# Kernel tuning notes

Hardware: AMD Instinct MI355X
Metric: run time of the kernel (lower is better)

Reference implementation:

```python
import jax, jax.numpy as jnp
import numpy as np

N_NODES = 50000
N_EDGES = 800000
IN_DIM = 256
HIDDEN = 64
HEADS = 4
LATENT = 128


def setup_inputs() -> dict:
    key = jax.random.key(0)
    ks = jax.random.split(key, 16)
    def p(k, shape, scale=0.05):
        return jax.random.normal(k, shape, jnp.float32) * scale
    d = {}
    d["x"] = jax.random.normal(ks[0], (N_NODES, IN_DIM), jnp.float32)
    d["edge_index"] = jax.random.randint(ks[1], (2, N_EDGES), 0, N_NODES)
    d["w_in"] = p(ks[2], (IN_DIM, HIDDEN)); d["b_in"] = jnp.zeros((HIDDEN,), jnp.float32)
    # GAT layer 0: in=HIDDEN, out=HIDDEN, heads=HEADS, concat
    d["W0"] = p(ks[3], (HIDDEN, HEADS * HIDDEN))
    d["as0"] = p(ks[4], (HEADS, HIDDEN)); d["ad0"] = p(ks[5], (HEADS, HIDDEN))
    d["bb0"] = jnp.zeros((HEADS * HIDDEN,), jnp.float32)
    # GAT layer 1: in=HEADS*HIDDEN, out=HIDDEN, heads=HEADS, concat
    d["W1"] = p(ks[6], (HEADS * HIDDEN, HEADS * HIDDEN))
    d["as1"] = p(ks[7], (HEADS, HIDDEN)); d["ad1"] = p(ks[8], (HEADS, HIDDEN))
    d["bb1"] = jnp.zeros((HEADS * HIDDEN,), jnp.float32)
    # GAT layer 2: in=HEADS*HIDDEN, out=HIDDEN, heads=1, concat=False
    d["W2"] = p(ks[9], (HEADS * HIDDEN, HIDDEN))
    d["as2"] = p(ks[10], (1, HIDDEN)); d["ad2"] = p(ks[11], (1, HIDDEN))
    d["bb2"] = jnp.zeros((HIDDEN,), jnp.float32)
    d["w_out"] = p(ks[12], (HIDDEN, LATENT)); d["b_out"] = jnp.zeros((LATENT,), jnp.float32)
    return d


def _gat(h, src, dst, W, a_s, a_d, b, concat, n):
    """PyG-style GATConv (eval mode, self-loops already appended to src/dst)."""
    heads, out = a_s.shape
    x = (h @ W).reshape(n, heads, out)                       # (N, H, D)
    e_src = jnp.einsum('nhd,hd->nh', x, a_s)                 # (N, H)
    e_dst = jnp.einsum('nhd,hd->nh', x, a_d)
    e = jax.nn.leaky_relu(e_src[src] + e_dst[dst], 0.2)      # (E, H)
    m = jax.ops.segment_max(e, dst, num_segments=n)          # segment-softmax over incoming edges
    w = jnp.exp(e - m[dst])
    s = jax.ops.segment_sum(w, dst, num_segments=n)
    alpha = w / s[dst]                                       # (E, H)
    agg = jax.ops.segment_sum(x[src] * alpha[:, :, None], dst, num_segments=n)  # (N, H, D)
    o = agg.reshape(n, heads * out) if concat else agg.mean(axis=1)
    return o + b


def reference(x, edge_index, w_in, b_in, W0, as0, ad0, bb0, W1, as1, ad1, bb1,
              W2, as2, ad2, bb2, w_out, b_out):
    n = x.shape[0]
    loop = jnp.arange(n)
    src = jnp.concatenate([edge_index[0], loop])   # add self-loops (PyG default)
    dst = jnp.concatenate([edge_index[1], loop])
    h = jax.nn.elu(x @ w_in + b_in)
    h = jax.nn.elu(_gat(h, src, dst, W0, as0, ad0, bb0, True, n))
    h = jax.nn.elu(_gat(h, src, dst, W1, as1, ad1, bb1, True, n))
    h = jax.nn.elu(_gat(h, src, dst, W2, as2, ad2, bb2, False, n))
    g = h.mean(axis=0, keepdims=True)              # batch=None -> global mean pool
    return g @ w_out + b_out                       # (1, LATENT)
```

## Files before the change

kernel.cpp:

```cpp
#include <hip/hip_runtime.h>

#define NN 50000
#define NE 800000
#define ET 850000
#define NAGG1 3125
#define MEGA_W    448
#define SCALL 3321
#define MEGA_GRID (SCALL + MEGA_W + 1)
#define GM64 782
#define GM128 391
#define PAD 64

#define HAS_FP8 1

typedef unsigned short ushort_t;
typedef unsigned int uint_t;
typedef __attribute__((ext_vector_type(8))) short short8;
typedef __attribute__((ext_vector_type(4))) float f32x4;
typedef __attribute__((ext_vector_type(2))) float f32x2;

__device__ __forceinline__ float elu1(float x) {
    return x > 0.f ? x : (__expf(x) - 1.f);
}
__device__ __forceinline__ float bf2f(ushort_t u) {
    return __uint_as_float(((uint_t)u) << 16);
}
__device__ __forceinline__ ushort_t f2bf(float f) {
    uint_t u = __float_as_uint(f);
    u += 0x7FFFu + ((u >> 16) & 1u);
    return (ushort_t)(u >> 16);
}
__device__ __forceinline__ uint_t pack2(float a, float b) {
    return (uint_t)f2bf(a) | ((uint_t)f2bf(b) << 16);
}
__device__ __forceinline__ void gl_lds16(const ushort_t* g, ushort_t* l) {
    __builtin_amdgcn_global_load_lds((const __attribute__((address_space(1))) void*)g,
                                     (__attribute__((address_space(3))) void*)l,
                                     16, 0, 0);
}
#define ACC2(q, w) do { \
    a0 += (w) * __uint_as_float((q).x << 16); \
    a1 += (w) * __uint_as_float((q).x & 0xFFFF0000u); \
    a2 += (w) * __uint_as_float((q).y << 16); \
    a3 += (w) * __uint_as_float((q).y & 0xFFFF0000u); } while (0)

__global__ void k_mega(const float* __restrict__ w_in, const float* __restrict__ W0,
                       const float* __restrict__ W1, const float* __restrict__ W2,
                       ushort_t* __restrict__ wiT, ushort_t* __restrict__ w0T,
                       ushort_t* __restrict__ w1T, ushort_t* __restrict__ w2T,
                       const int* __restrict__ ei, int* __restrict__ cursor,
                       int* __restrict__ pcsr,
                       float* __restrict__ gsum, int* __restrict__ tcount,
                       const float* __restrict__ as0, const float* __restrict__ ad0,
                       float* __restrict__ esA, float* __restrict__ edA) {
    int b = blockIdx.x, t = threadIdx.x;
    if (b < SCALL) {
        int e = b * 256 + t;
        if (e < ET) {
            int s, d;
            if (e < NE) { s = ei[e]; d = ei[NE + e]; }
            else        { s = d = e - NE; }
            int pos = atomicAdd(&cursor[d], 1);
            if (pos < PAD) pcsr[(d << 6) + pos] = s;
        }
    } else if (b < SCALL + MEGA_W) {
        int bw = b - SCALL;
        if (bw == 0 && t < 64) gsum[t] = 0.f;
        if (bw == 0 && t == 64) *tcount = 0;
        int i = bw * 256 + t;
        const float* W; ushort_t* Bt; int K, N, j;
        if (i < 16384)       { W = w_in; Bt = wiT; K = 256; N = 64;  j = i; }
        else if (i < 32768)  { W = W0;   Bt = w0T; K = 64;  N = 256; j = i - 16384; }
        else if (i < 98304)  { W = W1;   Bt = w1T; K = 256; N = 256; j = i - 32768; }
        else                 { W = W2;   Bt = w2T; K = 256; N = 64;  j = i - 98304; }
        int k = j / N, n = j % N;
        int jj = n & 63;
        int rp = (n & ~63) | ((jj & 3) << 4) | (jj >> 2);
        Bt[(size_t)rp * K + k] = f2bf(W[j]);
    } else {
        int h = t >> 6, k = t & 63;
        float ss = 0.f, sd = 0.f;
        for (int j = 0; j < 64; j++) {
            float w = W0[(size_t)k * 256 + h * 64 + j];
            ss += w * as0[h * 64 + j];
            sd += w * ad0[h * 64 + j];
        }
        esA[h * 64 + k] = ss;
        edA[h * 64 + k] = sd;
    }
}

template<bool ELU, bool BIAS, int NED, int MT, int NT, bool AF32, bool C8>
__device__ __forceinline__ void gemm_body(const void* __restrict__ Av,
                                          const ushort_t* __restrict__ Bt,
                                          const float* __restrict__ bias,
                                          ushort_t* __restrict__ C,
                                          const float* __restrict__ a_s,
                                          const float* __restrict__ a_d,
                                          float* __restrict__ es,
                                          float* __restrict__ ed,
                                          int esStride, int M, int K, int N,
                                          int bx, int by, int lda, int aoff) {
    constexpr int HG = NT / 4;
    constexpr int NEDC = (NED > 0) ? NED : 1;
    constexpr int BOFF = MT * 4096;
    __shared__ __align__(16) ushort_t lds[MT * 4096 + NT * 1024];
    int tid = threadIdx.x;
    int wave = tid >> 6, lane = tid & 63;
    int quad = lane >> 4, l16 = lane & 15;
    int mb = bx * (64 * MT), nb = by * (16 * NT);

    f32x4 acc[MT][NT];
    #pragma unroll
    for (int mt = 0; mt < MT; mt++)
        #pragma unroll
        for (int nt = 0; nt < NT; nt++)
            acc[mt][nt] = (f32x4){0.f, 0.f, 0.f, 0.f};

    for (int k0 = 0; k0 < K; k0 += 64) {
        #pragma unroll
        for (int c = 0; c < NT / 2; c++) {
            int id = wave * (NT / 2) + c;
            int ntile = id % NT;
            int ks = id / NT;
            int n = nb + ntile * 16 + l16;
            int col = k0 + ks * 32 + quad * 8;
            gl_lds16(Bt + (size_t)n * K + col,
                     &lds[BOFF + (ntile * 2 + ks) * 512]);
        }
        #pragma unroll
        for (int c = 0; c < 2 * MT; c++) {
            int mt = (MT == 2) ? (wave * 2 + (c >> 1)) : wave;
            int ks = (MT == 2) ? (c & 1) : c;
            int row = mb + mt * 16 + l16;
            row = min(row, M - 1);
            int col = k0 + ks * 32 + quad * 8;
            if constexpr (AF32) {
                const float* Af = (const float*)Av;
                float4 v0 = *(const float4*)(Af + (size_t)row * lda + aoff + col);
                float4 v1 = *(const float4*)(Af + (size_t)row * lda + aoff + col + 4);
                uint4 pk;
                pk.x = pack2(v0.x, v0.y); pk.y = pack2(v0.z, v0.w);
                pk.z = pack2(v1.x, v1.y); pk.w = pack2(v1.z, v1.w);
                *(uint4*)&lds[(mt * 2 + ks) * 512 + lane * 8] = pk;
            } else {
                gl_lds16((const ushort_t*)Av + (size_t)row * lda + aoff + col,
                         &lds[(mt * 2 + ks) * 512]);
            }
        }
        __syncthreads();
        #pragma unroll
        for (int ks = 0; ks < 2; ks++) {
            short8 af[MT];
            #pragma unroll
            for (int mt = 0; mt < MT; mt++)
                af[mt] = *(const short8*)&lds[((wave * MT + mt) * 2 + ks) * 512 + lane * 8];
            short8 bf[NT];
            #pragma unroll
            for (int nt = 0; nt < NT; nt++)
                bf[nt] = *(const short8*)&lds[BOFF + (nt * 2 + ks) * 512 + lane * 8];
            #pragma unroll
            for (int mt = 0; mt < MT; mt++)
                #pragma unroll
                for (int nt = 0; nt < NT; nt++)
                    acc[mt][nt] = __builtin_amdgcn_mfma_f32_16x16x32_bf16(
                        af[mt], bf[nt], acc[mt][nt], 0, 0, 0);
        }
        __syncthreads();
    }
    float4 as4[HG * NEDC], ad4[HG * NEDC], b4[HG];
    #pragma unroll
    for (int hg = 0; hg < HG; hg++) {
        int cbase = nb + hg * 64 + l16 * 4;
        if constexpr (NED > 0) {
            #pragma unroll
            for (int nd = 0; nd < NED; nd++) {
                as4[hg * NED + nd] = *(const float4*)(a_s + (size_t)((by * HG + hg) * NED + nd) * 64 + l16 * 4);
                ad4[hg * NED + nd] = *(const float4*)(a_d + (size_t)((by * HG + hg) * NED + nd) * 64 + l16 * 4);
            }
        }
        if (BIAS) b4[hg] = *(const float4*)(bias + cbase);
    }
    #pragma unroll
    for (int mt = 0; mt < MT; mt++) {
        int mrow = mb + (wave * MT + mt) * 16 + quad * 4;
        #pragma unroll
        for (int r = 0; r < 4; r++) {
            int m = mrow + r;
            bool mv = m < M;
            #pragma unroll
            for (int hg = 0; hg < HG; hg++) {
                float v0 = acc[mt][hg * 4 + 0][r];
                float v1 = acc[mt][hg * 4 + 1][r];
                float v2 = acc[mt][hg * 4 + 2][r];
                float v3 = acc[mt][hg * 4 + 3][r];
                if (BIAS) { v0 += b4[hg].x; v1 += b4[hg].y; v2 += b4[hg].z; v3 += b4[hg].w; }
                if (ELU) { v0 = elu1(v0); v1 = elu1(v1); v2 = elu1(v2); v3 = elu1(v3); }
                if constexpr (NED > 0) {
                    float ps[NED], pd[NED];
                    #pragma unroll
                    for (int nd = 0; nd < NED; nd++) {
                        ps[nd] = v0 * as4[hg * NED + nd].x + v1 * as4[hg * NED + nd].y
                               + v2 * as4[hg * NED + nd].z + v3 * as4[hg * NED + nd].w;
                        pd[nd] = v0 * ad4[hg * NED + nd].x + v1 * ad4[hg * NED + nd].y
                               + v2 * ad4[hg * NED + nd].z + v3 * ad4[hg * NED + nd].w;
                    }
                    #pragma unroll
                    for (int o = 8; o >= 1; o >>= 1)
                        #pragma unroll
                        for (int nd = 0; nd < NED; nd++) {
                            ps[nd] += __shfl_xor(ps[nd], o, 64);
                            pd[nd] += __shfl_xor(pd[nd], o, 64);
                        }
                    if (l16 == 0 && mv) {
                        #pragma unroll
                        for (int nd = 0; nd < NED; nd++) {
                            int head = (by * HG + hg) * NED + nd;
                            es[(size_t)m * esStride + head] = ps[nd];
                            ed[(size_t)m * esStride + head] = pd[nd];
                        }
                    }
                }
                if (mv) {
                    if constexpr (C8) {
#if HAS_FP8
                        int r8 = __builtin_amdgcn_cvt_pk_fp8_f32(v0, v1, 0, false);
                        r8 = __builtin_amdgcn_cvt_pk_fp8_f32(v2, v3, r8, true);
                        *(uint_t*)&((unsigned char*)C)[(size_t)m * N + nb + hg * 64 + l16 * 4] = (uint_t)r8;
#endif
                    } else {
                        ushort4 o;
                        o.x = f2bf(v0); o.y = f2bf(v1); o.z = f2bf(v2); o.w = f2bf(v3);
                        *(ushort4*)&C[(size_t)m * N + nb + hg * 64 + l16 * 4] = o;
                    }
                }
            }
        }
    }
}

template<bool ELU, bool BIAS, int NED, int MT, int NT, bool C8>
__global__ __launch_bounds__(256) void gemm_mfma(const ushort_t* __restrict__ A,
                                                 const ushort_t* __restrict__ Bt,
                                                 const float* __restrict__ bias,
                                                 ushort_t* __restrict__ C,
                                                 const float* __restrict__ a_s,
                                                 const float* __restrict__ a_d,
                                                 float* __restrict__ es,
                                                 float* __restrict__ ed,
                                                 int esStride, int M, int K, int N) {
    gemm_body<ELU, BIAS, NED, MT, NT, false, C8>(A, Bt, bias, C, a_s, a_d, es, ed,
                                                 esStride, M, K, N, blockIdx.x, blockIdx.y,
                                                 K, 0);
}

__global__ __launch_bounds__(256) void gemm_w0(const ushort_t* __restrict__ A,
                                               const ushort_t* __restrict__ Bt,
                                               const float* __restrict__ bias,
                                               ushort_t* __restrict__ C) {
    gemm_body<true, true, 0, 1, 4, false, false>(A, Bt, bias, C, nullptr, nullptr,
                                                 nullptr, nullptr, 0, NN, 64, 256,
                                                 blockIdx.x, blockIdx.y, 256,
                                                 blockIdx.y * 64);
}

__global__ __launch_bounds__(256) void k_gin(const float* __restrict__ x,
                                             const ushort_t* __restrict__ Bt,
                                             const float* __restrict__ bias,
                                             ushort_t* __restrict__ C,
                                             const float* __restrict__ esA,
                                             const float* __restrict__ edA,
                                             float* __restrict__ es,
                                             float* __restrict__ ed) {
    gemm_body<true, true, 4, 1, 4, true, true>(x, Bt, bias, C, esA, edA,
                                               es, ed, 4, NN, 256, 64,
                                               blockIdx.x, 0, 256, 0);
}

#define AGGH_STEP(T) do { \
    int s_ = __shfl(idx, (T) + eo, 64); \
    float4 w4_ = *(const float4*)&wlds[wave][((T) + eo) * 4]; \
    uint_t q_ = xq[(size_t)s_ * 16 + l16]; \
    f32x2 lo_ = __builtin_amdgcn_cvt_pk_f32_fp8((int)q_, false); \
    f32x2 hi_ = __builtin_amdgcn_cvt_pk_f32_fp8((int)q_, true); \
    float f0_ = lo_.x, f1_ = lo_.y, f2_ = hi_.x, f3_ = hi_.y; \
    acc[0][0] += w4_.x * f0_; acc[0][1] += w4_.x * f1_; \
    acc[0][2] += w4_.x * f2_; acc[0][3] += w4_.x * f3_; \
    acc[1][0] += w4_.y * f0_; acc[1][1] += w4_.y * f1_; \
    acc[1][2] += w4_.y * f2_; acc[1][3] += w4_.y * f3_; \
    acc[2][0] += w4_.z * f0_; acc[2][1] += w4_.z * f1_; \
    acc[2][2] += w4_.z * f2_; acc[2][3] += w4_.z * f3_; \
    acc[3][0] += w4_.w * f0_; acc[3][1] += w4_.w * f1_; \
    acc[3][2] += w4_.w * f2_; acc[3][3] += w4_.w * f3_; \
} while (0)

__global__ __launch_bounds__(256) void k_aggH(const void* __restrict__ xl,
                                              const float* __restrict__ es,
                                              const float* __restrict__ ed,
                                              const int* __restrict__ degv,
                                              const int* __restrict__ pcsr,
                                              ushort_t* __restrict__ outv) {
    __shared__ float wlds[4][256];
    int lane = threadIdx.x & 63, wave = threadIdx.x >> 6;
    int node = blockIdx.x * 4 + wave;
    if (node >= NN) return;
    int eo = lane >> 4, l16 = lane & 15;
    int deg = min(degv[node], PAD);
    int nb = node << 6;
    float4 edv = *(const float4*)(ed + (size_t)node * 4);
    float edh[4] = {edv.x, edv.y, edv.z, edv.w};
    float acc[4][4];
    #pragma unroll
    for (int h = 0; h < 4; h++)
        #pragma unroll
        for (int j = 0; j < 4; j++) acc[h][j] = 0.f;
    const uint_t* xq = (const uint_t*)xl;

    bool valid = lane < deg;
    int idx = pcsr[nb + (valid ? lane : 0)];
    float4 ev = *(const float4*)(es + (size_t)idx * 4);
    float e[4] = {ev.x, ev.y, ev.z, ev.w};
    #pragma unroll
    for (int h = 0; h < 4; h++) {
        float v = e[h] + edh[h];
        v = v > 0.f ? v : 0.2f * v;
        e[h] = valid ? v : -1e30f;
    }
    float cm[4];
    #pragma unroll
    for (int h = 0; h < 4; h++) cm[h] = e[h];
    #pragma unroll
    for (int o = 32; o >= 1; o >>= 1)
        #pragma unroll
        for (int h = 0; h < 4; h++) cm[h] = fmaxf(cm[h], __shfl_xor(cm[h], o, 64));
    float cs[4];
    #pragma unroll
    for (int h = 0; h < 4; h++) cs[h] = valid ? __expf(e[h] - cm[h]) : 0.f;
    #pragma unroll
    for (int o = 32; o >= 1; o >>= 1)
        #pragma unroll
        for (int h = 0; h < 4; h++) cs[h] += __shfl_xor(cs[h], o, 64);
    float4 wv;
    wv.x = valid ? __expf(e[0] - cm[0]) / cs[0] : 0.f;
    wv.y = valid ? __expf(e[1] - cm[1]) / cs[1] : 0.f;
    wv.z = valid ? __expf(e[2] - cm[2]) / cs[2] : 0.f;
    wv.w = valid ? __expf(e[3] - cm[3]) / cs[3] : 0.f;
    *(float4*)&wlds[wave][lane * 4] = wv;
    int t = 0;
    for (; t + 8 <= deg; t += 8) { AGGH_STEP(t); AGGH_STEP(t + 4); }
    for (; t < deg; t += 4) AGGH_STEP(t);

    #pragma unroll
    for (int h = 0; h < 4; h++)
        #pragma unroll
        for (int j = 0; j < 4; j++) {
            acc[h][j] += __shfl_xor(acc[h][j], 16, 64);
            acc[h][j] += __shfl_xor(acc[h][j], 32, 64);
        }
    float r0 = eo == 0 ? acc[0][0] : eo == 1 ? acc[1][0] : eo == 2 ? acc[2][0] : acc[3][0];
    float r1 = eo == 0 ? acc[0][1] : eo == 1 ? acc[1][1] : eo == 2 ? acc[2][1] : acc[3][1];
    float r2 = eo == 0 ? acc[0][2] : eo == 1 ? acc[1][2] : eo == 2 ? acc[2][2] : acc[3][2];
    float r3 = eo == 0 ? acc[0][3] : eo == 1 ? acc[1][3] : eo == 2 ? acc[2][3] : acc[3][3];
    ushort4 o;
    o.x = f2bf(r0); o.y = f2bf(r1); o.z = f2bf(r2); o.w = f2bf(r3);
    *(ushort4*)(outv + (size_t)node * 256 + lane * 4) = o;
}

template<bool BFOUT, bool F8IN>
__global__ __launch_bounds__(256) void k_agg4(const void* __restrict__ xl,
                                              const float* __restrict__ es,
                                              const float* __restrict__ ed,
                                              const int* __restrict__ degv,
                                              const int* __restrict__ pcsr,
                                              const float* __restrict__ bias,
                                              void* __restrict__ outv) {
    __shared__ float wlds[4][256];
    int lane = threadIdx.x & 63, wave = threadIdx.x >> 6;
    int node = blockIdx.x * 4 + wave;
    if (node >= NN) return;
    int head = lane >> 4;
    int deg = min(degv[node], PAD);
    int nb = node << 6;
    float4 edv = *(const float4*)(ed + (size_t)node * 4);
    float edh[4] = {edv.x, edv.y, edv.z, edv.w};
    float a0 = 0.f, a1 = 0.f, a2 = 0.f, a3 = 0.f;

    bool valid = lane < deg;
    int idx = pcsr[nb + (valid ? lane : 0)];
    float4 ev = *(const float4*)(es + (size_t)idx * 4);
    float e[4] = {ev.x, ev.y, ev.z, ev.w};
    #pragma unroll
    for (int h = 0; h < 4; h++) {
        float v = e[h] + edh[h];
        v = v > 0.f ? v : 0.2f * v;
        e[h] = valid ? v : -1e30f;
    }
    float cm[4];
    #pragma unroll
    for (int h = 0; h < 4; h++) cm[h] = e[h];
    #pragma unroll
    for (int o = 32; o >= 1; o >>= 1)
        #pragma unroll
        for (int h = 0; h < 4; h++) cm[h] = fmaxf(cm[h], __shfl_xor(cm[h], o, 64));
    float cs[4];
    #pragma unroll
    for (int h = 0; h < 4; h++) cs[h] = valid ? __expf(e[h] - cm[h]) : 0.f;
    #pragma unroll
    for (int o = 32; o >= 1; o >>= 1)
        #pragma unroll
        for (int h = 0; h < 4; h++) cs[h] += __shfl_xor(cs[h], o, 64);
    float4 wv;
    wv.x = valid ? __expf(e[0] - cm[0]) / cs[0] : 0.f;
    wv.y = valid ? __expf(e[1] - cm[1]) / cs[1] : 0.f;
    wv.z = valid ? __expf(e[2] - cm[2]) / cs[2] : 0.f;
    wv.w = valid ? __expf(e[3] - cm[3]) / cs[3] : 0.f;
    *(float4*)&wlds[wave][lane * 4] = wv;

    if constexpr (F8IN) {
#if HAS_FP8
        const uint_t* xq = (const uint_t*)xl;
        int t = 0;
        for (; t + 4 <= deg; t += 4) {
            int s0 = __shfl(idx, t + 0, 64), s1 = __shfl(idx, t + 1, 64);
            int s2 = __shfl(idx, t + 2, 64), s3 = __shfl(idx, t + 3, 64);
            uint_t q0 = xq[(size_t)s0 * 64 + lane];
            uint_t q1 = xq[(size_t)s1 * 64 + lane];
            uint_t q2 = xq[(size_t)s2 * 64 + lane];
            uint_t q3 = xq[(size_t)s3 * 64 + lane];
            float w0 = wlds[wave][(t + 0) * 4 + head], w1 = wlds[wave][(t + 1) * 4 + head];
            float w2 = wlds[wave][(t + 2) * 4 + head], w3 = wlds[wave][(t + 3) * 4 + head];
            f32x2 lo, hi;
            lo = __builtin_amdgcn_cvt_pk_f32_fp8((int)q0, false);
            hi = __builtin_amdgcn_cvt_pk_f32_fp8((int)q0, true);
            a0 += w0 * lo.x; a1 += w0 * lo.y; a2 += w0 * hi.x; a3 += w0 * hi.y;
            lo = __builtin_amdgcn_cvt_pk_f32_fp8((int)q1, false);
            hi = __builtin_amdgcn_cvt_pk_f32_fp8((int)q1, true);
            a0 += w1 * lo.x; a1 += w1 * lo.y; a2 += w1 * hi.x; a3 += w1 * hi.y;
            lo = __builtin_amdgcn_cvt_pk_f32_fp8((int)q2, false);
            hi = __builtin_amdgcn_cvt_pk_f32_fp8((int)q2, true);
            a0 += w2 * lo.x; a1 += w2 * lo.y; a2 += w2 * hi.x; a3 += w2 * hi.y;
            lo = __builtin_amdgcn_cvt_pk_f32_fp8((int)q3, false);
            hi = __builtin_amdgcn_cvt_pk_f32_fp8((int)q3, true);
            a0 += w3 * lo.x; a1 += w3 * lo.y; a2 += w3 * hi.x; a3 += w3 * hi.y;
        }
        for (; t < deg; ++t) {
            int s0 = __shfl(idx, t, 64);
            uint_t q0 = xq[(size_t)s0 * 64 + lane];
            float w0 = wlds[wave][t * 4 + head];
            f32x2 lo = __builtin_amdgcn_cvt_pk_f32_fp8((int)q0, false);
            f32x2 hi = __builtin_amdgcn_cvt_pk_f32_fp8((int)q0, true);
            a0 += w0 * lo.x; a1 += w0 * lo.y; a2 += w0 * hi.x; a3 += w0 * hi.y;
        }
#endif
    } else {
        const uint_t* xb = (const uint_t*)xl;
        int t = 0;
        for (; t + 4 <= deg; t += 4) {
            int s0 = __shfl(idx, t + 0, 64), s1 = __shfl(idx, t + 1, 64);
            int s2 = __shfl(idx, t + 2, 64), s3 = __shfl(idx, t + 3, 64);
            uint2 q0 = *(const uint2*)(xb + (size_t)s0 * 128 + lane * 2);
            uint2 q1 = *(const uint2*)(xb + (size_t)s1 * 128 + lane * 2);
            uint2 q2 = *(const uint2*)(xb + (size_t)s2 * 128 + lane * 2);
            uint2 q3 = *(const uint2*)(xb + (size_t)s3 * 128 + lane * 2);
            float w0 = wlds[wave][(t + 0) * 4 + head], w1 = wlds[wave][(t + 1) * 4 + head];
            float w2 = wlds[wave][(t + 2) * 4 + head], w3 = wlds[wave][(t + 3) * 4 + head];
            ACC2(q0, w0); ACC2(q1, w1); ACC2(q2, w2); ACC2(q3, w3);
        }
        for (; t < deg; ++t) {
            int s0 = __shfl(idx, t, 64);
            uint2 q0 = *(const uint2*)(xb + (size_t)s0 * 128 + lane * 2);
            float w0 = wlds[wave][t * 4 + head];
            ACC2(q0, w0);
        }
    }

    float o0 = elu1(a0 + bias[lane * 4 + 0]);
    float o1 = elu1(a1 + bias[lane * 4 + 1]);
    float o2 = elu1(a2 + bias[lane * 4 + 2]);
    float o3 = elu1(a3 + bias[lane * 4 + 3]);
    if constexpr (BFOUT) {
        ushort4 o; o.x = f2bf(o0); o.y = f2bf(o1); o.z = f2bf(o2); o.w = f2bf(o3);
        *(ushort4*)((ushort_t*)outv + (size_t)node * 256 + lane * 4) = o;
    } else {
        float4 o; o.x = o0; o.y = o1; o.z = o2; o.w = o3;
        *(float4*)((float*)outv + (size_t)node * 256 + lane * 4) = o;
    }
}

__global__ __launch_bounds__(256) void k_agg1(const void* __restrict__ xl,
                                              const float* __restrict__ es,
                                              const float* __restrict__ ed,
                                              const int* __restrict__ degv,
                                              const int* __restrict__ pcsr,
                                              const float* __restrict__ bias,
                                              float* __restrict__ part) {
    __shared__ float wlds[4][64];
    __shared__ float ps[4][64];
    int lane = threadIdx.x & 63, wave = threadIdx.x >> 6;
    int g = lane >> 4, l16 = lane & 15;
    int node = blockIdx.x * 16 + wave * 4 + g;
    bool vn = node < NN;
    int deg = vn ? min(degv[node], PAD) : 0;
    int nb = node << 6;
    float edl = vn ? ed[node] : 0.f;

    float m = -1e30f, ssum = 0.f;
    for (int base = 0; base < deg; base += 16) {
        int i = base + l16;
        bool valid = i < deg;
        int idx = pcsr[nb + (valid ? i : 0)];
        float e = es[idx] + edl;
        e = e > 0.f ? e : 0.2f * e;
        e = valid ? e : -1e30f;
        float cm = e;
        #pragma unroll
        for (int o = 8; o >= 1; o >>= 1) cm = fmaxf(cm, __shfl_xor(cm, o, 64));
        float cs = valid ? __expf(e - cm) : 0.f;
        #pragma unroll
        for (int o = 8; o >= 1; o >>= 1) cs += __shfl_xor(cs, o, 64);
        float mn = fmaxf(m, cm);
        ssum = ssum * __expf(m - mn) + cs * __expf(cm - mn);
        m = mn;
    }
    float inv = 1.f / ssum;

    float a0 = 0.f, a1 = 0.f, a2 = 0.f, a3 = 0.f;
    const uint_t* xq = (const uint_t*)xl;
    for (int base = 0; base < deg; base += 16) {
        int i = base + l16;
        bool valid = i < deg;
        int idx = pcsr[nb + (valid ? i : 0)];
        int cnt = min(16, deg - base);
        float e = es[idx] + edl;
        e = e > 0.f ? e : 0.2f * e;
        wlds[wave][g * 16 + l16] = valid ? __expf(e - m) * inv : 0.f;
        int t = 0;
        for (; t + 4 <= cnt; t += 4) {
            int s0 = __shfl(idx, g * 16 + t + 0, 64), s1 = __shfl(idx, g * 16 + t + 1, 64);
            int s2 = __shfl(idx, g * 16 + t + 2, 64), s3 = __shfl(idx, g * 16 + t + 3, 64);
            uint_t q0 = xq[(size_t)s0 * 16 + l16];
            uint_t q1 = xq[(size_t)s1 * 16 + l16];
            uint_t q2 = xq[(size_t)s2 * 16 + l16];
            uint_t q3 = xq[(size_t)s3 * 16 + l16];
            float w0 = wlds[wave][g * 16 + t + 0], w1 = wlds[wave][g * 16 + t + 1];
            float w2 = wlds[wave][g * 16 + t + 2], w3 = wlds[wave][g * 16 + t + 3];
            f32x2 lo, hi;
            lo = __builtin_amdgcn_cvt_pk_f32_fp8((int)q0, false);
            hi = __builtin_amdgcn_cvt_pk_f32_fp8((int)q0, true);
            a0 += w0 * lo.x; a1 += w0 * lo.y; a2 += w0 * hi.x; a3 += w0 * hi.y;
            lo = __builtin_amdgcn_cvt_pk_f32_fp8((int)q1, false);
            hi = __builtin_amdgcn_cvt_pk_f32_fp8((int)q1, true);
            a0 += w1 * lo.x; a1 += w1 * lo.y; a2 += w1 * hi.x; a3 += w1 * hi.y;
            lo = __builtin_amdgcn_cvt_pk_f32_fp8((int)q2, false);
            hi = __builtin_amdgcn_cvt_pk_f32_fp8((int)q2, true);
            a0 += w2 * lo.x; a1 += w2 * lo.y; a2 += w2 * hi.x; a3 += w2 * hi.y;
            lo = __builtin_amdgcn_cvt_pk_f32_fp8((int)q3, false);
            hi = __builtin_amdgcn_cvt_pk_f32_fp8((int)q3, true);
            a0 += w3 * lo.x; a1 += w3 * lo.y; a2 += w3 * hi.x; a3 += w3 * hi.y;
        }
        for (; t < cnt; ++t) {
            int s = __shfl(idx, g * 16 + t, 64);
            float w = wlds[wave][g * 16 + t];
            uint_t q = xq[(size_t)s * 16 + l16];
            f32x2 lo = __builtin_amdgcn_cvt_pk_f32_fp8((int)q, false);
            f32x2 hi = __builtin_amdgcn_cvt_pk_f32_fp8((int)q, true);
            a0 += w * lo.x; a1 += w * lo.y; a2 += w * hi.x; a3 += w * hi.y;
        }
    }

    float o[4];
    o[0] = vn ? elu1(a0 + bias[l16 * 4 + 0]) : 0.f;
    o[1] = vn ? elu1(a1 + bias[l16 * 4 + 1]) : 0.f;
    o[2] = vn ? elu1(a2 + bias[l16 * 4 + 2]) : 0.f;
    o[3] = vn ? elu1(a3 + bias[l16 * 4 + 3]) : 0.f;
    #pragma unroll
    for (int j = 0; j < 4; j++) {
        o[j] += __shfl_xor(o[j], 16, 64);
        o[j] += __shfl_xor(o[j], 32, 64);
    }
    if (lane < 16) {
        float4 v; v.x = o[0]; v.y = o[1]; v.z = o[2]; v.w = o[3];
        *(float4*)&ps[wave][l16 * 4] = v;
    }
    __syncthreads();
    int tid = threadIdx.x;
    if (tid < 64) {
        float tot = ps[0][tid] + ps[1][tid] + ps[2][tid] + ps[3][tid];
        part[(size_t)blockIdx.x * 64 + tid] = tot;
    }
}

__global__ void k_red(const float* __restrict__ part, float* __restrict__ gsum,
                      int* __restrict__ tcount, const float* __restrict__ w_out,
                      const float* __restrict__ b_out, float* __restrict__ out) {
    __shared__ float sm[4][64];
    __shared__ float gs[64];
    __shared__ int lastFlag;
    int t = threadIdx.x, c = t & 63, w = t >> 6;
    float s = 0.f;
    for (int r = blockIdx.x * 4 + w; r < NAGG1; r += gridDim.x * 4)
        s += part[(size_t)r * 64 + c];
    sm[w][c] = s;
    __syncthreads();
    if (w == 0) {
        float tot = sm[0][c] + sm[1][c] + sm[2][c] + sm[3][c];
        atomicAdd(&gsum[c], tot);
    }
    if (t == 0) {
        __threadfence();
        lastFlag = (atomicAdd(tcount, 1) == 63);
    }
    __syncthreads();
    if (!lastFlag) return;
    if (t < 64)
        gs[t] = __hip_atomic_load(&gsum[t], __ATOMIC_ACQUIRE, __HIP_MEMORY_SCOPE_AGENT);
    __syncthreads();
    if (t < 128) {
        float acc = b_out[t];
        const float invn = 1.f / (float)NN;
        #pragma unroll 8
        for (int k = 0; k < 64; k++)
            acc += (gs[k] * invn) * w_out[k * 128 + t];
        out[t] = acc;
    }
}

extern "C" void kernel_launch(void* const* d_in, const int* in_sizes, int n_in,
                              void* d_out, int out_size, void* d_ws, size_t ws_size,
                              hipStream_t stream) {
    const float* x    = (const float*)d_in[0];
    const int*   ei   = (const int*)d_in[1];
    const float* w_in = (const float*)d_in[2];
    const float* b_in = (const float*)d_in[3];
    const float* W0   = (const float*)d_in[4];
    const float* as0  = (const float*)d_in[5];
    const float* ad0  = (const float*)d_in[6];
    const float* bb0  = (const float*)d_in[7];
    const float* W1   = (const float*)d_in[8];
    const float* as1  = (const float*)d_in[9];
    const float* ad1  = (const float*)d_in[10];
    const float* bb1  = (const float*)d_in[11];
    const float* W2   = (const float*)d_in[12];
    const float* as2  = (const float*)d_in[13];
    const float* ad2  = (const float*)d_in[14];
    const float* bb2  = (const float*)d_in[15];
    const float* w_out= (const float*)d_in[16];
    const float* b_out= (const float*)d_in[17];
    float* out = (float*)d_out;

    char* p = (char*)d_ws;
    size_t off = 0;
    auto take = [&](size_t bytes) {
        char* r = p + off;
        off = (off + bytes + 255) & ~(size_t)255;
        return r;
    };
    ushort_t* h0b    = (ushort_t*)take((size_t)NN * 64 * 2);
    ushort_t* xl_bf  = (ushort_t*)take((size_t)NN * 256 * 2);
    ushort_t* hb_bf  = (ushort_t*)take((size_t)NN * 256 * 2);
    ushort_t* h2_bf  = (ushort_t*)take((size_t)NN * 64 * 2);
    ushort_t* wiT    = (ushort_t*)take((size_t)64 * 512 * 2);
    ushort_t* w0T    = (ushort_t*)take((size_t)256 * 128 * 2);
    ushort_t* w1T    = (ushort_t*)take((size_t)256 * 512 * 2);
    ushort_t* w2T    = (ushort_t*)take((size_t)64 * 512 * 2);
    float*    es     = (float*)take((size_t)NN * 4 * 4);
    float*    ed     = (float*)take((size_t)NN * 4 * 4);
    int*      cursor = (int*)take((size_t)NN * 4);
    int*      pcsr   = (int*)take((size_t)NN * PAD * 4);
    float*    part   = (float*)take((size_t)NAGG1 * 64 * 4);
    float*    gsum   = (float*)take(64 * 4);
    int*      tcount = (int*)take(4);
    float*    esA    = (float*)take(256 * 4);
    float*    edA    = (float*)take(256 * 4);
    unsigned char* x1f8 = (unsigned char*)xl_bf;
    unsigned char* h0f8 = (unsigned char*)h0b;
    unsigned char* h2f8 = (unsigned char*)h2_bf;

    hipMemsetAsync(cursor, 0, (size_t)NN * 4, stream);

    k_mega<<<MEGA_GRID, 256, 0, stream>>>(w_in, W0, W1, W2, wiT, w0T, w1T, w2T,
                                          ei, cursor, pcsr, gsum, tcount,
                                          as0, ad0, esA, edA);

    k_gin<<<GM64, 256, 0, stream>>>(x, wiT, b_in, (ushort_t*)h0f8, esA, edA, es, ed);

    k_aggH<<<(NN + 3) / 4, 256, 0, stream>>>(h0f8, es, ed, cursor, pcsr, xl_bf);
    gemm_w0<<<dim3(GM64, 4), 256, 0, stream>>>(xl_bf, w0T, bb0, hb_bf);

    gemm_mfma<false, false, 1, 2, 8, true><<<dim3(GM128, 2), 256, 0, stream>>>(
        hb_bf, w1T, nullptr, (ushort_t*)x1f8, as1, ad1, es, ed, 4, NN, 256, 256);
    k_agg4<true, true><<<(NN + 3) / 4, 256, 0, stream>>>(x1f8, es, ed, cursor, pcsr, bb1, hb_bf);

    gemm_mfma<false, false, 1, 1, 4, true><<<dim3(GM64, 1), 256, 0, stream>>>(
        hb_bf, w2T, nullptr, (ushort_t*)h2f8, as2, ad2, es, ed, 1, NN, 256, 64);
    k_agg1<<<NAGG1, 256, 0, stream>>>(h2f8, es, ed, cursor, pcsr, bb2, part);

    k_red<<<64, 256, 0, stream>>>(part, gsum, tcount, w_out, b_out, out);
}
```

Before: 361.0 us.

## Synthesize self-loops in aggregation kernels and use packed f32x2 FMA accumulation

Self-loop edges are no longer scattered into the padded CSR with atomics. Each aggregation kernel now appends the node itself as an implicit final neighbour, which removes 50k atomic inserts and the extra scatter blocks. The accumulation loops in the three aggregation kernels are rewritten with two-wide float vectors so the compiler can emit packed FMA instructions. The unused bf16-input path of k_agg4 is removed, and the per-node neighbour cap drops by one to leave room for the self-loop.

New measurement: 356.2 us. No clear change (-1.3%).

```diff
diff --git a/kernel.cpp b/kernel.cpp
--- a/kernel.cpp
+++ b/kernel.cpp
@@ -2,10 +2,9 @@
 
 #define NN 50000
 #define NE 800000
-#define ET 850000
 #define NAGG1 3125
 #define MEGA_W    448
-#define SCALL 3321
+#define SCALL 3125
 #define MEGA_GRID (SCALL + MEGA_W + 1)
 #define GM64 782
 #define GM128 391
@@ -38,11 +37,6 @@
                                      (__attribute__((address_space(3))) void*)l,
                                      16, 0, 0);
 }
-#define ACC2(q, w) do { \
-    a0 += (w) * __uint_as_float((q).x << 16); \
-    a1 += (w) * __uint_as_float((q).x & 0xFFFF0000u); \
-    a2 += (w) * __uint_as_float((q).y << 16); \
-    a3 += (w) * __uint_as_float((q).y & 0xFFFF0000u); } while (0)
 
 __global__ void k_mega(const float* __restrict__ w_in, const float* __restrict__ W0,
                        const float* __restrict__ W1, const float* __restrict__ W2,
@@ -56,12 +50,10 @@
     int b = blockIdx.x, t = threadIdx.x;
     if (b < SCALL) {
         int e = b * 256 + t;
-        if (e < ET) {
-            int s, d;
-            if (e < NE) { s = ei[e]; d = ei[NE + e]; }
-            else        { s = d = e - NE; }
+        if (e < NE) {
+            int s = ei[e], d = ei[NE + e];
             int pos = atomicAdd(&cursor[d], 1);
-            if (pos < PAD) pcsr[(d << 6) + pos] = s;
+            if (pos < PAD - 1) pcsr[(d << 6) + pos] = s;
         }
     } else if (b < SCALL + MEGA_W) {
         int bw = b - SCALL;
@@ -283,15 +275,12 @@
     uint_t q_ = xq[(size_t)s_ * 16 + l16]; \
     f32x2 lo_ = __builtin_amdgcn_cvt_pk_f32_fp8((int)q_, false); \
     f32x2 hi_ = __builtin_amdgcn_cvt_pk_f32_fp8((int)q_, true); \
-    float f0_ = lo_.x, f1_ = lo_.y, f2_ = hi_.x, f3_ = hi_.y; \
-    acc[0][0] += w4_.x * f0_; acc[0][1] += w4_.x * f1_; \
-    acc[0][2] += w4_.x * f2_; acc[0][3] += w4_.x * f3_; \
-    acc[1][0] += w4_.y * f0_; acc[1][1] += w4_.y * f1_; \
-    acc[1][2] += w4_.y * f2_; acc[1][3] += w4_.y * f3_; \
-    acc[2][0] += w4_.z * f0_; acc[2][1] += w4_.z * f1_; \
-    acc[2][2] += w4_.z * f2_; acc[2][3] += w4_.z * f3_; \
-    acc[3][0] += w4_.w * f0_; acc[3][1] += w4_.w * f1_; \
-    acc[3][2] += w4_.w * f2_; acc[3][3] += w4_.w * f3_; \
+    f32x2 wx_ = (f32x2){w4_.x, w4_.x}, wy_ = (f32x2){w4_.y, w4_.y}; \
+    f32x2 wz_ = (f32x2){w4_.z, w4_.z}, ww_ = (f32x2){w4_.w, w4_.w}; \
+    accv[0][0] += wx_ * lo_; accv[0][1] += wx_ * hi_; \
+    accv[1][0] += wy_ * lo_; accv[1][1] += wy_ * hi_; \
+    accv[2][0] += wz_ * lo_; accv[2][1] += wz_ * hi_; \
+    accv[3][0] += ww_ * lo_; accv[3][1] += ww_ * hi_; \
 } while (0)
 
 __global__ __launch_bounds__(256) void k_aggH(const void* __restrict__ xl,
@@ -305,19 +294,21 @@
     int node = blockIdx.x * 4 + wave;
     if (node >= NN) return;
     int eo = lane >> 4, l16 = lane & 15;
-    int deg = min(degv[node], PAD);
+    int degr = min(degv[node], PAD - 1);
+    int deg = degr + 1;
     int nb = node << 6;
     float4 edv = *(const float4*)(ed + (size_t)node * 4);
     float edh[4] = {edv.x, edv.y, edv.z, edv.w};
-    float acc[4][4];
-    #pragma unroll
-    for (int h = 0; h < 4; h++)
-        #pragma unroll
-        for (int j = 0; j < 4; j++) acc[h][j] = 0.f;
+    f32x2 accv[4][2];
+    #pragma unroll
+    for (int h = 0; h < 4; h++) {
+        accv[h][0] = (f32x2){0.f, 0.f};
+        accv[h][1] = (f32x2){0.f, 0.f};
+    }
     const uint_t* xq = (const uint_t*)xl;
 
     bool valid = lane < deg;
-    int idx = pcsr[nb + (valid ? lane : 0)];
+    int idx = (lane < degr) ? pcsr[nb + lane] : node;
     float4 ev = *(const float4*)(es + (size_t)idx * 4);
     float e[4] = {ev.x, ev.y, ev.z, ev.w};
     #pragma unroll
@@ -350,6 +341,12 @@
     for (; t + 8 <= deg; t += 8) { AGGH_STEP(t); AGGH_STEP(t + 4); }
     for (; t < deg; t += 4) AGGH_STEP(t);
 
+    float acc[4][4];
+    #pragma unroll
+    for (int h = 0; h < 4; h++) {
+        acc[h][0] = accv[h][0].x; acc[h][1] = accv[h][0].y;
+        acc[h][2] = accv[h][1].x; acc[h][3] = accv[h][1].y;
+    }
     #pragma unroll
     for (int h = 0; h < 4; h++)
         #pragma unroll
@@ -366,7 +363,14 @@
     *(ushort4*)(outv + (size_t)node * 256 + lane * 4) = o;
 }
 
-template<bool BFOUT, bool F8IN>
+#define AGG4_EDGE(Q, W) do { \
+    f32x2 lo = __builtin_amdgcn_cvt_pk_f32_fp8((int)(Q), false); \
+    f32x2 hi = __builtin_amdgcn_cvt_pk_f32_fp8((int)(Q), true); \
+    f32x2 ws = (f32x2){(W), (W)}; \
+    a01 += ws * lo; a23 += ws * hi; \
+} while (0)
+
+template<bool BFOUT>
 __global__ __launch_bounds__(256) void k_agg4(const void* __restrict__ xl,
                                               const float* __restrict__ es,
                                               const float* __restrict__ ed,
@@ -379,14 +383,15 @@
     int node = blockIdx.x * 4 + wave;
     if (node >= NN) return;
     int head = lane >> 4;
-    int deg = min(degv[node], PAD);
+    int degr = min(degv[node], PAD - 1);
+    int deg = degr + 1;
     int nb = node << 6;
     float4 edv = *(const float4*)(ed + (size_t)node * 4);
     float edh[4] = {edv.x, edv.y, edv.z, edv.w};
-    float a0 = 0.f, a1 = 0.f, a2 = 0.f, a3 = 0.f;
+    f32x2 a01 = (f32x2){0.f, 0.f}, a23 = (f32x2){0.f, 0.f};
 
     bool valid = lane < deg;
-    int idx = pcsr[nb + (valid ? lane : 0)];
+    int idx = (lane < degr) ? pcsr[nb + lane] : node;
     float4 ev = *(const float4*)(es + (size_t)idx * 4);
     float e[4] = {ev.x, ev.y, ev.z, ev.w};
     #pragma unroll
@@ -416,68 +421,32 @@
     wv.w = valid ? __expf(e[3] - cm[3]) / cs[3] : 0.f;
     *(float4*)&wlds[wave][lane * 4] = wv;
 
-    if constexpr (F8IN) {
 #if HAS_FP8
-        const uint_t* xq = (const uint_t*)xl;
-        int t = 0;
-        for (; t + 4 <= deg; t += 4) {
-            int s0 = __shfl(idx, t + 0, 64), s1 = __shfl(idx, t + 1, 64);
-            int s2 = __shfl(idx, t + 2, 64), s3 = __shfl(idx, t + 3, 64);
-            uint_t q0 = xq[(size_t)s0 * 64 + lane];
-            uint_t q1 = xq[(size_t)s1 * 64 + lane];
-            uint_t q2 = xq[(size_t)s2 * 64 + lane];
-            uint_t q3 = xq[(size_t)s3 * 64 + lane];
-            float w0 = wlds[wave][(t + 0) * 4 + head], w1 = wlds[wave][(t + 1) * 4 + head];
-            float w2 = wlds[wave][(t + 2) * 4 + head], w3 = wlds[wave][(t + 3) * 4 + head];
-            f32x2 lo, hi;
-            lo = __builtin_amdgcn_cvt_pk_f32_fp8((int)q0, false);
-            hi = __builtin_amdgcn_cvt_pk_f32_fp8((int)q0, true);
-            a0 += w0 * lo.x; a1 += w0 * lo.y; a2 += w0 * hi.x; a3 += w0 * hi.y;
-            lo = __builtin_amdgcn_cvt_pk_f32_fp8((int)q1, false);
-            hi = __builtin_amdgcn_cvt_pk_f32_fp8((int)q1, true);
-            a0 += w1 * lo.x; a1 += w1 * lo.y; a2 += w1 * hi.x; a3 += w1 * hi.y;
-            lo = __builtin_amdgcn_cvt_pk_f32_fp8((int)q2, false);
-            hi = __builtin_amdgcn_cvt_pk_f32_fp8((int)q2, true);
-            a0 += w2 * lo.x; a1 += w2 * lo.y; a2 += w2 * hi.x; a3 += w2 * hi.y;
-            lo = __builtin_amdgcn_cvt_pk_f32_fp8((int)q3, false);
-            hi = __builtin_amdgcn_cvt_pk_f32_fp8((int)q3, true);
-            a0 += w3 * lo.x; a1 += w3 * lo.y; a2 += w3 * hi.x; a3 += w3 * hi.y;
-        }
-        for (; t < deg; ++t) {
-            int s0 = __shfl(idx, t, 64);
-            uint_t q0 = xq[(size_t)s0 * 64 + lane];
-            float w0 = wlds[wave][t * 4 + head];
-            f32x2 lo = __builtin_amdgcn_cvt_pk_f32_fp8((int)q0, false);
-            f32x2 hi = __builtin_amdgcn_cvt_pk_f32_fp8((int)q0, true);
-            a0 += w0 * lo.x; a1 += w0 * lo.y; a2 += w0 * hi.x; a3 += w0 * hi.y;
-        }
+    const uint_t* xq = (const uint_t*)xl;
+    int t = 0;
+    for (; t + 4 <= deg; t += 4) {
+        int s0 = __shfl(idx, t + 0, 64), s1 = __shfl(idx, t + 1, 64);
+        int s2 = __shfl(idx, t + 2, 64), s3 = __shfl(idx, t + 3, 64);
+        uint_t q0 = xq[(size_t)s0 * 64 + lane];
+        uint_t q1 = xq[(size_t)s1 * 64 + lane];
+        uint_t q2 = xq[(size_t)s2 * 64 + lane];
+        uint_t q3 = xq[(size_t)s3 * 64 + lane];
+        float w0 = wlds[wave][(t + 0) * 4 + head], w1 = wlds[wave][(t + 1) * 4 + head];
+        float w2 = wlds[wave][(t + 2) * 4 + head], w3 = wlds[wave][(t + 3) * 4 + head];
+        AGG4_EDGE(q0, w0); AGG4_EDGE(q1, w1); AGG4_EDGE(q2, w2); AGG4_EDGE(q3, w3);
+    }
+    for (; t < deg; ++t) {
+        int s0 = __shfl(idx, t, 64);
+        uint_t q0 = xq[(size_t)s0 * 64 + lane];
+        float w0 = wlds[wave][t * 4 + head];
+        AGG4_EDGE(q0, w0);
+    }
 #endif
-    } else {
-        const uint_t* xb = (const uint_t*)xl;
-        int t = 0;
-        for (; t + 4 <= deg; t += 4) {
-            int s0 = __shfl(idx, t + 0, 64), s1 = __shfl(idx, t + 1, 64);
-            int s2 = __shfl(idx, t + 2, 64), s3 = __shfl(idx, t + 3, 64);
-            uint2 q0 = *(const uint2*)(xb + (size_t)s0 * 128 + lane * 2);
-            uint2 q1 = *(const uint2*)(xb + (size_t)s1 * 128 + lane * 2);
-            uint2 q2 = *(const uint2*)(xb + (size_t)s2 * 128 + lane * 2);
-            uint2 q3 = *(const uint2*)(xb + (size_t)s3 * 128 + lane * 2);
-            float w0 = wlds[wave][(t + 0) * 4 + head], w1 = wlds[wave][(t + 1) * 4 + head];
-            float w2 = wlds[wave][(t + 2) * 4 + head], w3 = wlds[wave][(t + 3) * 4 + head];
-            ACC2(q0, w0); ACC2(q1, w1); ACC2(q2, w2); ACC2(q3, w3);
-        }
-        for (; t < deg; ++t) {
-            int s0 = __shfl(idx, t, 64);
-            uint2 q0 = *(const uint2*)(xb + (size_t)s0 * 128 + lane * 2);
-            float w0 = wlds[wave][t * 4 + head];
-            ACC2(q0, w0);
-        }
-    }
-
-    float o0 = elu1(a0 + bias[lane * 4 + 0]);
-    float o1 = elu1(a1 + bias[lane * 4 + 1]);
-    float o2 = elu1(a2 + bias[lane * 4 + 2]);
-    float o3 = elu1(a3 + bias[lane * 4 + 3]);
+
+    float o0 = elu1(a01.x + bias[lane * 4 + 0]);
+    float o1 = elu1(a01.y + bias[lane * 4 + 1]);
+    float o2 = elu1(a23.x + bias[lane * 4 + 2]);
+    float o3 = elu1(a23.y + bias[lane * 4 + 3]);
     if constexpr (BFOUT) {
         ushort4 o; o.x = f2bf(o0); o.y = f2bf(o1); o.z = f2bf(o2); o.w = f2bf(o3);
         *(ushort4*)((ushort_t*)outv + (size_t)node * 256 + lane * 4) = o;
@@ -500,7 +469,8 @@
     int g = lane >> 4, l16 = lane & 15;
     int node = blockIdx.x * 16 + wave * 4 + g;
     bool vn = node < NN;
-    int deg = vn ? min(degv[node], PAD) : 0;
+    int degr = vn ? min(degv[node], PAD - 1) : 0;
+    int deg = vn ? degr + 1 : 0;
     int nb = node << 6;
     float edl = vn ? ed[node] : 0.f;
 
@@ -508,7 +478,7 @@
     for (int base = 0; base < deg; base += 16) {
         int i = base + l16;
         bool valid = i < deg;
-        int idx = pcsr[nb + (valid ? i : 0)];
+        int idx = (i < degr) ? pcsr[nb + i] : node;
         float e = es[idx] + edl;
         e = e > 0.f ? e : 0.2f * e;
         e = valid ? e : -1e30f;
@@ -524,12 +494,12 @@
     }
     float inv = 1.f / ssum;
 
-    float a0 = 0.f, a1 = 0.f, a2 = 0.f, a3 = 0.f;
+    f32x2 a01 = (f32x2){0.f, 0.f}, a23 = (f32x2){0.f, 0.f};
     const uint_t* xq = (const uint_t*)xl;
     for (int base = 0; base < deg; base += 16) {
         int i = base + l16;
         bool valid = i < deg;
-        int idx = pcsr[nb + (valid ? i : 0)];
+        int idx = (i < degr) ? pcsr[nb + i] : node;
         int cnt = min(16, deg - base);
         float e = es[idx] + edl;
         e = e > 0.f ? e : 0.2f * e;
@@ -544,35 +514,21 @@
             uint_t q3 = xq[(size_t)s3 * 16 + l16];
             float w0 = wlds[wave][g * 16 + t + 0], w1 = wlds[wave][g * 16 + t + 1];
             float w2 = wlds[wave][g * 16 + t + 2], w3 = wlds[wave][g * 16 + t + 3];
-            f32x2 lo, hi;
-            lo = __builtin_amdgcn_cvt_pk_f32_fp8((int)q0, false);
-            hi = __builtin_amdgcn_cvt_pk_f32_fp8((int)q0, true);
-            a0 += w0 * lo.x; a1 += w0 * lo.y; a2 += w0 * hi.x; a3 += w0 * hi.y;
-            lo = __builtin_amdgcn_cvt_pk_f32_fp8((int)q1, false);
-            hi = __builtin_amdgcn_cvt_pk_f32_fp8((int)q1, true);
-            a0 += w1 * lo.x; a1 += w1 * lo.y; a2 += w1 * hi.x; a3 += w1 * hi.y;
-            lo = __builtin_amdgcn_cvt_pk_f32_fp8((int)q2, false);
-            hi = __builtin_amdgcn_cvt_pk_f32_fp8((int)q2, true);
-            a0 += w2 * lo.x; a1 += w2 * lo.y; a2 += w2 * hi.x; a3 += w2 * hi.y;
-            lo = __builtin_amdgcn_cvt_pk_f32_fp8((int)q3, false);
-            hi = __builtin_amdgcn_cvt_pk_f32_fp8((int)q3, true);
-            a0 += w3 * lo.x; a1 += w3 * lo.y; a2 += w3 * hi.x; a3 += w3 * hi.y;
+            AGG4_EDGE(q0, w0); AGG4_EDGE(q1, w1); AGG4_EDGE(q2, w2); AGG4_EDGE(q3, w3);
         }
         for (; t < cnt; ++t) {
             int s = __shfl(idx, g * 16 + t, 64);
             float w = wlds[wave][g * 16 + t];
             uint_t q = xq[(size_t)s * 16 + l16];
-            f32x2 lo = __builtin_amdgcn_cvt_pk_f32_fp8((int)q, false);
-            f32x2 hi = __builtin_amdgcn_cvt_pk_f32_fp8((int)q, true);
-            a0 += w * lo.x; a1 += w * lo.y; a2 += w * hi.x; a3 += w * hi.y;
+            AGG4_EDGE(q, w);
         }
     }
 
     float o[4];
-    o[0] = vn ? elu1(a0 + bias[l16 * 4 + 0]) : 0.f;
-    o[1] = vn ? elu1(a1 + bias[l16 * 4 + 1]) : 0.f;
-    o[2] = vn ? elu1(a2 + bias[l16 * 4 + 2]) : 0.f;
-    o[3] = vn ? elu1(a3 + bias[l16 * 4 + 3]) : 0.f;
+    o[0] = vn ? elu1(a01.x + bias[l16 * 4 + 0]) : 0.f;
+    o[1] = vn ? elu1(a01.y + bias[l16 * 4 + 1]) : 0.f;
+    o[2] = vn ? elu1(a23.x + bias[l16 * 4 + 2]) : 0.f;
+    o[3] = vn ? elu1(a23.y + bias[l16 * 4 + 3]) : 0.f;
     #pragma unroll
     for (int j = 0; j < 4; j++) {
         o[j] += __shfl_xor(o[j], 16, 64);
@@ -689,7 +645,7 @@
 
     gemm_mfma<false, false, 1, 2, 8, true><<<dim3(GM128, 2), 256, 0, stream>>>(
         hb_bf, w1T, nullptr, (ushort_t*)x1f8, as1, ad1, es, ed, 4, NN, 256, 256);
-    k_agg4<true, true><<<(NN + 3) / 4, 256, 0, stream>>>(x1f8, es, ed, cursor, pcsr, bb1, hb_bf);
+    k_agg4<true><<<(NN + 3) / 4, 256, 0, stream>>>(x1f8, es, ed, cursor, pcsr, bb1, hb_bf);
 
     gemm_mfma<false, false, 1, 1, 4, true><<<dim3(GM64, 1), 256, 0, stream>>>(
         hb_bf, w2T, nullptr, (ushort_t*)h2f8, as2, ad2, es, ed, 1, NN, 256, 64);
```
